# Performance work log

Hardware: AMD Instinct MI355X
Metric: run time of the kernel (lower is better)

## Reference

```python
import jax, jax.numpy as jnp
import numpy as np

N_EMBD = 1024
N_HEAD = 16
HEAD_DIM = N_EMBD // N_HEAD
B, T = 2, 2048


def setup_inputs() -> dict:
    key = jax.random.key(0)
    k1, k2, k3 = jax.random.split(key, 3)
    s_in = 1.0 / np.sqrt(N_EMBD)
    return {
        "x": jax.random.normal(k1, (B, T, N_EMBD), dtype=jnp.float32),
        "w_qkv": jax.random.normal(k2, (N_EMBD, 3 * N_EMBD), dtype=jnp.float32) * s_in,
        "b_qkv": jnp.zeros((3 * N_EMBD,), dtype=jnp.float32),
        "w_out": jax.random.normal(k3, (N_EMBD, N_EMBD), dtype=jnp.float32) * s_in,
        "b_out": jnp.zeros((N_EMBD,), dtype=jnp.float32),
    }


def reference(x, w_qkv, b_qkv, w_out, b_out):
    b, t, c = x.shape
    qkv = x @ w_qkv + b_qkv  # [B,T,3C]
    q, k, v = jnp.split(qkv, 3, axis=-1)
    # [B,T,C] -> [B,H,T,D]
    reshape = lambda a: a.reshape(b, t, N_HEAD, HEAD_DIM).transpose(0, 2, 1, 3)
    q, k, v = reshape(q), reshape(k), reshape(v)
    scale = 1.0 / jnp.sqrt(jnp.asarray(HEAD_DIM, dtype=x.dtype))
    att = jnp.einsum("bhqd,bhkd->bhqk", q, k) * scale  # [B,H,T,T]
    causal = jnp.tril(jnp.ones((t, t), dtype=bool))
    att = jnp.where(causal, att, jnp.asarray(-jnp.inf, dtype=att.dtype))
    att = jax.nn.softmax(att, axis=-1)
    y = jnp.einsum("bhqk,bhkd->bhqd", att, v)  # [B,H,T,D]
    y = y.transpose(0, 2, 1, 3).reshape(b, t, c)
    return y @ w_out + b_out
```

## Files before the change

### kernel.cpp

```cpp
#include <hip/hip_runtime.h>

typedef unsigned short u16;
typedef __attribute__((ext_vector_type(8))) short s16x8;
typedef __attribute__((ext_vector_type(8))) unsigned short u16x8;
typedef __attribute__((ext_vector_type(4))) unsigned short u16x4;
typedef __attribute__((ext_vector_type(4))) float f32x4;

__device__ __forceinline__ u16 f2bf(float f) {
  unsigned int u = __float_as_uint(f);
  u += 0x7fffu + ((u >> 16) & 1u);
  return (u16)(u >> 16);
}

__device__ __forceinline__ void gload_lds16(const u16* g, u16* l) {
  __builtin_amdgcn_global_load_lds((__attribute__((address_space(1))) void*)(u16*)g,
                                   (__attribute__((address_space(3))) void*)l, 16, 0, 0);
}

__global__ void __launch_bounds__(256) prep_kernel(const float* __restrict__ x,
                                                   u16* __restrict__ xbf,
                                                   const float* __restrict__ wqkv,
                                                   u16* __restrict__ wqkvT,
                                                   const float* __restrict__ wout,
                                                   u16* __restrict__ woutT) {
  __shared__ float tile[32][33];
  const int b = blockIdx.x, tid = threadIdx.x;
  if (b < 2048) {
    int i = (b * 256 + tid) * 8;
    float4 a = *(const float4*)(x + i);
    float4 c = *(const float4*)(x + i + 4);
    u16x8 o;
    o[0] = f2bf(a.x); o[1] = f2bf(a.y); o[2] = f2bf(a.z); o[3] = f2bf(a.w);
    o[4] = f2bf(c.x); o[5] = f2bf(c.y); o[6] = f2bf(c.z); o[7] = f2bf(c.w);
    *(u16x8*)(xbf + i) = o;
    return;
  }
  const float* in; u16* out; int K = 1024, N, bx, by;
  if (b < 5120) { in = wqkv; out = wqkvT; N = 3072; bx = (b - 2048) % 96; by = (b - 2048) / 96; }
  else          { in = wout; out = woutT; N = 1024; bx = (b - 5120) % 32; by = (b - 5120) / 32; }
  int n0 = bx * 32, k0 = by * 32;
  int r = tid >> 5, c = tid & 31;
#pragma unroll
  for (int i = 0; i < 4; ++i)
    tile[r + i * 8][c] = in[(size_t)(k0 + r + i * 8) * N + n0 + c];
  __syncthreads();
#pragma unroll
  for (int i = 0; i < 4; ++i)
    out[(size_t)(n0 + r + i * 8) * K + k0 + c] = f2bf(tile[c][r + i * 8]);
}

__device__ __forceinline__ void gemm_core(const u16* __restrict__ A,
                                          const u16* __restrict__ BT, int K,
                                          int m0, int n0, u16* As, u16* Bs,
                                          f32x4 acc[4][4]) {
  const int tid = threadIdx.x;
  const int lane = tid & 63, wave = tid >> 6;
  const int quad = lane >> 4, l16 = lane & 15;
  const int wm = (wave & 1) << 6, wn = (wave >> 1) << 6;
  const int ob0 = wave * 2048 + lane * 16;
  const int ob1 = ob0 + 1024;
  const int r0 = ob0 >> 6, c0 = (ob0 & 63) >> 1;
  const int r1 = ob1 >> 6, c1 = (ob1 & 63) >> 1;

  for (int k0 = 0; k0 < K; k0 += 32) {
    __syncthreads();
    gload_lds16(&A [(size_t)(m0 + r0) * K + k0 + c0], &As[ob0 >> 1]);
    gload_lds16(&A [(size_t)(m0 + r1) * K + k0 + c1], &As[ob1 >> 1]);
    gload_lds16(&BT[(size_t)(n0 + r0) * K + k0 + c0], &Bs[ob0 >> 1]);
    gload_lds16(&BT[(size_t)(n0 + r1) * K + k0 + c1], &Bs[ob1 >> 1]);
    __syncthreads();
    s16x8 a[4], b[4];
#pragma unroll
    for (int i = 0; i < 4; ++i)
      a[i] = *(const s16x8*)&As[(wm + i * 16 + l16) * 32 + quad * 8];
#pragma unroll
    for (int j = 0; j < 4; ++j)
      b[j] = *(const s16x8*)&Bs[(wn + j * 16 + l16) * 32 + quad * 8];
#pragma unroll
    for (int i = 0; i < 4; ++i)
#pragma unroll
      for (int j = 0; j < 4; ++j)
        acc[i][j] = __builtin_amdgcn_mfma_f32_16x16x32_bf16(a[i], b[j], acc[i][j], 0, 0, 0);
  }
}

__global__ void __launch_bounds__(256) gemm_qkv_kernel(const u16* __restrict__ xbf,
                                                       const u16* __restrict__ wT,
                                                       const float* __restrict__ bias,
                                                       u16* __restrict__ qb,
                                                       u16* __restrict__ kb,
                                                       u16* __restrict__ vtb) {
  __shared__ u16 As[128 * 32], Bs[128 * 32];
  f32x4 acc[4][4];
#pragma unroll
  for (int i = 0; i < 4; ++i)
#pragma unroll
    for (int j = 0; j < 4; ++j) { f32x4 z = {0.f, 0.f, 0.f, 0.f}; acc[i][j] = z; }
  const int m0 = blockIdx.x * 128, n0 = blockIdx.y * 128;
  gemm_core(xbf, wT, 1024, m0, n0, As, Bs, acc);

  const int tid = threadIdx.x;
  const int lane = tid & 63, wave = tid >> 6;
  const int quad = lane >> 4, l16 = lane & 15;
  const int wm = (wave & 1) << 6, wn = (wave >> 1) << 6;
  const int sec = n0 >> 10;
#pragma unroll
  for (int i = 0; i < 4; ++i)
#pragma unroll
    for (int j = 0; j < 4; ++j) {
      const int gm = m0 + wm + i * 16 + quad * 4;
      const int gn = n0 + wn + j * 16 + l16;
      const float bv = bias[gn];
      const int c = gn & 1023, h = c >> 6, d = c & 63;
#pragma unroll
      for (int r = 0; r < 4; ++r) {
        const int row = gm + r;
        const int bb = row >> 11, t = row & 2047;
        if (sec == 0)      qb[((size_t)(bb * 16 + h) * 2048 + t) * 64 + d] = f2bf((acc[i][j][r] + bv) * 0.125f);
        else if (sec == 1) kb[((size_t)(bb * 16 + h) * 2048 + t) * 64 + d] = f2bf(acc[i][j][r] + bv);
        else               vtb[((size_t)(bb * 16 + h) * 64 + d) * 2048 + t] = f2bf(acc[i][j][r] + bv);
      }
    }
}

__global__ void __launch_bounds__(256) gemm_out_kernel(const u16* __restrict__ yb,
                                                       const u16* __restrict__ wT,
                                                       const float* __restrict__ bias,
                                                       float* __restrict__ out) {
  __shared__ u16 As[64 * 32], Bs[128 * 32];
  f32x4 acc[2][4];
#pragma unroll
  for (int i = 0; i < 2; ++i)
#pragma unroll
    for (int j = 0; j < 4; ++j) { f32x4 z = {0.f, 0.f, 0.f, 0.f}; acc[i][j] = z; }
  const int m0 = blockIdx.x * 64, n0 = blockIdx.y * 128;
  const int K = 1024;

  const int tid = threadIdx.x;
  const int lane = tid & 63, wave = tid >> 6;
  const int quad = lane >> 4, l16 = lane & 15;
  const int wm = (wave & 1) << 5, wn = (wave >> 1) << 6;
  const int oa = tid * 16;
  const int ra = oa >> 6, ca = (oa & 63) >> 1;
  const int ob0 = wave * 2048 + lane * 16;
  const int ob1 = ob0 + 1024;
  const int rb0 = ob0 >> 6, cb0 = (ob0 & 63) >> 1;
  const int rb1 = ob1 >> 6, cb1 = (ob1 & 63) >> 1;

  for (int k0 = 0; k0 < K; k0 += 32) {
    __syncthreads();
    gload_lds16(&yb[(size_t)(m0 + ra) * K + k0 + ca],  &As[oa >> 1]);
    gload_lds16(&wT[(size_t)(n0 + rb0) * K + k0 + cb0], &Bs[ob0 >> 1]);
    gload_lds16(&wT[(size_t)(n0 + rb1) * K + k0 + cb1], &Bs[ob1 >> 1]);
    __syncthreads();
    s16x8 a[2], b[4];
#pragma unroll
    for (int i = 0; i < 2; ++i)
      a[i] = *(const s16x8*)&As[(wm + i * 16 + l16) * 32 + quad * 8];
#pragma unroll
    for (int j = 0; j < 4; ++j)
      b[j] = *(const s16x8*)&Bs[(wn + j * 16 + l16) * 32 + quad * 8];
#pragma unroll
    for (int i = 0; i < 2; ++i)
#pragma unroll
      for (int j = 0; j < 4; ++j)
        acc[i][j] = __builtin_amdgcn_mfma_f32_16x16x32_bf16(a[i], b[j], acc[i][j], 0, 0, 0);
  }

#pragma unroll
  for (int i = 0; i < 2; ++i)
#pragma unroll
    for (int j = 0; j < 4; ++j) {
      const int gm = m0 + wm + i * 16 + quad * 4;
      const int gn = n0 + wn + j * 16 + l16;
      const float bv = bias[gn];
#pragma unroll
      for (int r = 0; r < 4; ++r)
        out[(size_t)(gm + r) * 1024 + gn] = acc[i][j][r] + bv;
    }
}

__global__ void __launch_bounds__(256) attn_kernel(const u16* __restrict__ qb,
                                                   const u16* __restrict__ kb,
                                                   const u16* __restrict__ vtb,
                                                   u16* __restrict__ yb) {
  const int KSTR = 72, VSTR = 136;
  __shared__ u16 Ks[128 * 72];
  __shared__ u16 VTs[64 * 136];
  __shared__ u16 Ps[4 * 16 * 136];

  const int p = blockIdx.x;
  const int bh = blockIdx.y;
  const int bb = bh >> 4, h = bh & 15;
  const u16* Q  = qb  + (size_t)bh * (2048 * 64);
  const u16* Km = kb  + (size_t)bh * (2048 * 64);
  const u16* VT = vtb + (size_t)bh * (64 * 2048);

  const int tid = threadIdx.x;
  const int wave = tid >> 6, lane = tid & 63;
  const int quad = lane >> 4, l16 = lane & 15;
  const float NINF = -__builtin_inff();
  const int Kr = tid >> 3, Kc = (tid & 7) * 8;
  const int Vr = tid >> 4, Vc = (tid & 15) * 8;
  u16* Pw = Ps + wave * (16 * 136);

  const int qtA = p, qtB = 31 - p;
  const int nktA = (qtA >> 1) + 1, nktB = (qtB >> 1) + 1;

  s16x8 qfA[2], qfB[2];
#pragma unroll
  for (int i = 0; i < 2; ++i) {
    int r = Kr + i * 32;
    *(u16x8*)&Ks[r * KSTR + Kc] = *(const u16x8*)&Q[(size_t)(qtA * 64 + r) * 64 + Kc];
  }
  __syncthreads();
#pragma unroll
  for (int ks = 0; ks < 2; ++ks)
    qfA[ks] = *(const s16x8*)&Ks[(wave * 16 + l16) * KSTR + ks * 32 + quad * 8];
  __syncthreads();
#pragma unroll
  for (int i = 0; i < 2; ++i) {
    int r = Kr + i * 32;
    *(u16x8*)&Ks[r * KSTR + Kc] = *(const u16x8*)&Q[(size_t)(qtB * 64 + r) * 64 + Kc];
  }
  __syncthreads();
#pragma unroll
  for (int ks = 0; ks < 2; ++ks)
    qfB[ks] = *(const s16x8*)&Ks[(wave * 16 + l16) * KSTR + ks * 32 + quad * 8];

  float lsumA = 0.f, lsumB = 0.f;
  f32x4 oaccA[4], oaccB[4];
#pragma unroll
  for (int dt = 0; dt < 4; ++dt) {
    f32x4 z = {0.f, 0.f, 0.f, 0.f};
    oaccA[dt] = z; oaccB[dt] = z;
  }

  u16x8 kv[4], vv[4];
#pragma unroll
  for (int i = 0; i < 4; ++i) {
    kv[i] = *(const u16x8*)&Km[(size_t)(Kr + i * 32) * 64 + Kc];
    vv[i] = *(const u16x8*)&VT[(size_t)(Vr + i * 16) * 2048 + Vc];
  }

  auto do_tile = [&](const s16x8 qf[2], int qt, int nkt, int kt,
                     float& lsum, f32x4 oacc[4]) {
    f32x4 st[2][4];
#pragma unroll
    for (int hh = 0; hh < 2; ++hh)
#pragma unroll
      for (int mt = 0; mt < 4; ++mt) {
        f32x4 z = {0.f, 0.f, 0.f, 0.f};
        s16x8 kf0 = *(const s16x8*)&Ks[(hh * 64 + mt * 16 + l16) * KSTR + quad * 8];
        s16x8 kf1 = *(const s16x8*)&Ks[(hh * 64 + mt * 16 + l16) * KSTR + 32 + quad * 8];
        z = __builtin_amdgcn_mfma_f32_16x16x32_bf16(kf0, qf[0], z, 0, 0, 0);
        st[hh][mt] = __builtin_amdgcn_mfma_f32_16x16x32_bf16(kf1, qf[1], z, 0, 0, 0);
      }
    if (kt == nkt - 1) {
      const int qrow = qt * 64 + wave * 16 + l16;
#pragma unroll
      for (int hh = 0; hh < 2; ++hh)
#pragma unroll
        for (int mt = 0; mt < 4; ++mt)
#pragma unroll
          for (int r = 0; r < 4; ++r) {
            int kcol = kt * 128 + hh * 64 + mt * 16 + quad * 4 + r;
            if (kcol > qrow) st[hh][mt][r] = NINF;
          }
    }
#pragma unroll
    for (int hh = 0; hh < 2; ++hh)
#pragma unroll
      for (int mt = 0; mt < 4; ++mt) {
        u16x4 pw;
#pragma unroll
        for (int r = 0; r < 4; ++r) {
          float e = __expf(st[hh][mt][r]);
          lsum += e;
          pw[r] = (u16)((__float_as_uint(e) + 0x8000u) >> 16);
        }
        *(u16x4*)&Pw[l16 * VSTR + hh * 64 + mt * 16 + quad * 4] = pw;
      }
#pragma unroll
    for (int kq = 0; kq < 4; ++kq) {
      s16x8 pf = *(const s16x8*)&Pw[l16 * VSTR + kq * 32 + quad * 8];
#pragma unroll
      for (int dt = 0; dt < 4; ++dt) {
        s16x8 vf = *(const s16x8*)&VTs[(dt * 16 + l16) * VSTR + kq * 32 + quad * 8];
        oacc[dt] = __builtin_amdgcn_mfma_f32_16x16x32_bf16(pf, vf, oacc[dt], 0, 0, 0);
      }
    }
  };

  for (int kt = 0; kt < nktB; ++kt) {
    __syncthreads();
#pragma unroll
    for (int i = 0; i < 4; ++i) {
      *(u16x8*)&Ks[(Kr + i * 32) * KSTR + Kc]  = kv[i];
      *(u16x8*)&VTs[(Vr + i * 16) * VSTR + Vc] = vv[i];
    }
    __syncthreads();
    if (kt + 1 < nktB) {
#pragma unroll
      for (int i = 0; i < 4; ++i) {
        kv[i] = *(const u16x8*)&Km[(size_t)((kt + 1) * 128 + Kr + i * 32) * 64 + Kc];
        vv[i] = *(const u16x8*)&VT[(size_t)(Vr + i * 16) * 2048 + (kt + 1) * 128 + Vc];
      }
    }
    do_tile(qfB, qtB, nktB, kt, lsumB, oaccB);
    if (kt < nktA) do_tile(qfA, qtA, nktA, kt, lsumA, oaccA);
  }

#pragma unroll
  for (int e = 0; e < 2; ++e) {
    const int qt = e ? qtB : qtA;
    float l = e ? lsumB : lsumA;
    f32x4* oacc = e ? oaccB : oaccA;
    l += __shfl_xor(l, 16, 64);
    l += __shfl_xor(l, 32, 64);
    float rinv[4];
#pragma unroll
    for (int r = 0; r < 4; ++r) rinv[r] = 1.0f / __shfl(l, quad * 4 + r, 64);
#pragma unroll
    for (int dt = 0; dt < 4; ++dt) {
      int d = dt * 16 + l16;
#pragma unroll
      for (int r = 0; r < 4; ++r) {
        int t = qt * 64 + wave * 16 + quad * 4 + r;
        yb[(((size_t)bb * 2048 + t) * 16 + h) * 64 + d] = f2bf(oacc[dt][r] * rinv[r]);
      }
    }
  }
}

extern "C" void kernel_launch(void* const* d_in, const int* in_sizes, int n_in,
                              void* d_out, int out_size, void* d_ws, size_t ws_size,
                              hipStream_t stream) {
  (void)in_sizes; (void)n_in; (void)out_size; (void)ws_size;
  const float* x    = (const float*)d_in[0];
  const float* wqkv = (const float*)d_in[1];
  const float* bqkv = (const float*)d_in[2];
  const float* wout = (const float*)d_in[3];
  const float* bout = (const float*)d_in[4];
  float* out = (float*)d_out;

  char* ws = (char*)d_ws;
  u16* xbf   = (u16*)(ws);
  u16* wqkvT = (u16*)(ws + (size_t)8  * 1024 * 1024);
  u16* woutT = (u16*)(ws + (size_t)14 * 1024 * 1024);
  u16* qb    = (u16*)(ws + (size_t)16 * 1024 * 1024);
  u16* kb    = (u16*)(ws + (size_t)24 * 1024 * 1024);
  u16* vtb   = (u16*)(ws + (size_t)32 * 1024 * 1024);
  u16* yb    = (u16*)(ws + (size_t)40 * 1024 * 1024);

  prep_kernel<<<6144, 256, 0, stream>>>(x, xbf, wqkv, wqkvT, wout, woutT);
  gemm_qkv_kernel<<<dim3(32, 24), 256, 0, stream>>>(xbf, wqkvT, bqkv, qb, kb, vtb);
  attn_kernel<<<dim3(16, 32), 256, 0, stream>>>(qb, kb, vtb, yb);
  gemm_out_kernel<<<dim3(64, 8), 256, 0, stream>>>(yb, woutT, bout, out);
}
```

Before: 195.0 us.

## Double K-step per barrier in GEMMs and split attention into sequential query passes

The QKV and output projection GEMMs now stage two 32-wide K slices per barrier pair, which halves the number of synchronisations and doubles LDS per block. The attention kernel no longer interleaves its two query tiles over a shared K/V stream. It processes each tile in its own pass, reloading K/V for the second, which lowers register pressure at the cost of re-reading shared K/V tiles from global memory. A stray assignment inside an MFMA argument is harmless but untidy.

Result: no change. 196.9 us (+0.9%).

```diff
diff --git a/kernel.cpp b/kernel.cpp
--- a/kernel.cpp
+++ b/kernel.cpp
@@ -61,26 +61,35 @@
   const int ob1 = ob0 + 1024;
   const int r0 = ob0 >> 6, c0 = (ob0 & 63) >> 1;
   const int r1 = ob1 >> 6, c1 = (ob1 & 63) >> 1;
-
-  for (int k0 = 0; k0 < K; k0 += 32) {
-    __syncthreads();
-    gload_lds16(&A [(size_t)(m0 + r0) * K + k0 + c0], &As[ob0 >> 1]);
-    gload_lds16(&A [(size_t)(m0 + r1) * K + k0 + c1], &As[ob1 >> 1]);
-    gload_lds16(&BT[(size_t)(n0 + r0) * K + k0 + c0], &Bs[ob0 >> 1]);
-    gload_lds16(&BT[(size_t)(n0 + r1) * K + k0 + c1], &Bs[ob1 >> 1]);
-    __syncthreads();
-    s16x8 a[4], b[4];
-#pragma unroll
-    for (int i = 0; i < 4; ++i)
-      a[i] = *(const s16x8*)&As[(wm + i * 16 + l16) * 32 + quad * 8];
-#pragma unroll
-    for (int j = 0; j < 4; ++j)
-      b[j] = *(const s16x8*)&Bs[(wn + j * 16 + l16) * 32 + quad * 8];
-#pragma unroll
-    for (int i = 0; i < 4; ++i)
+  const int CH = 128 * 32;
+
+  for (int k0 = 0; k0 < K; k0 += 64) {
+    __syncthreads();
+#pragma unroll
+    for (int kk = 0; kk < 2; ++kk) {
+      const int kg = k0 + kk * 32, co = kk * CH;
+      gload_lds16(&A [(size_t)(m0 + r0) * K + kg + c0], &As[co + (ob0 >> 1)]);
+      gload_lds16(&A [(size_t)(m0 + r1) * K + kg + c1], &As[co + (ob1 >> 1)]);
+      gload_lds16(&BT[(size_t)(n0 + r0) * K + kg + c0], &Bs[co + (ob0 >> 1)]);
+      gload_lds16(&BT[(size_t)(n0 + r1) * K + kg + c1], &Bs[co + (ob1 >> 1)]);
+    }
+    __syncthreads();
+#pragma unroll
+    for (int kk = 0; kk < 2; ++kk) {
+      const int co = kk * CH;
+      s16x8 a[4], b[4];
+#pragma unroll
+      for (int i = 0; i < 4; ++i)
+        a[i] = *(const s16x8*)&As[co + (wm + i * 16 + l16) * 32 + quad * 8];
 #pragma unroll
       for (int j = 0; j < 4; ++j)
-        acc[i][j] = __builtin_amdgcn_mfma_f32_16x16x32_bf16(a[i], b[j], acc[i][j], 0, 0, 0);
+        b[j] = *(const s16x8*)&Bs[co + (wn + j * 16 + l16) * 32 + quad * 8];
+#pragma unroll
+      for (int i = 0; i < 4; ++i)
+#pragma unroll
+        for (int j = 0; j < 4; ++j)
+          acc[i][j] = __builtin_amdgcn_mfma_f32_16x16x32_bf16(a[i], b[j], acc[i][j], 0, 0, 0);
+    }
   }
 }
 
@@ -90,7 +99,7 @@
                                                        u16* __restrict__ qb,
                                                        u16* __restrict__ kb,
                                                        u16* __restrict__ vtb) {
-  __shared__ u16 As[128 * 32], Bs[128 * 32];
+  __shared__ u16 As[2 * 128 * 32], Bs[2 * 128 * 32];
   f32x4 acc[4][4];
 #pragma unroll
   for (int i = 0; i < 4; ++i)
@@ -127,7 +136,7 @@
                                                        const u16* __restrict__ wT,
                                                        const float* __restrict__ bias,
                                                        float* __restrict__ out) {
-  __shared__ u16 As[64 * 32], Bs[128 * 32];
+  __shared__ u16 As[2 * 64 * 32], Bs[2 * 128 * 32];
   f32x4 acc[2][4];
 #pragma unroll
   for (int i = 0; i < 2; ++i)
@@ -146,25 +155,33 @@
   const int ob1 = ob0 + 1024;
   const int rb0 = ob0 >> 6, cb0 = (ob0 & 63) >> 1;
   const int rb1 = ob1 >> 6, cb1 = (ob1 & 63) >> 1;
-
-  for (int k0 = 0; k0 < K; k0 += 32) {
-    __syncthreads();
-    gload_lds16(&yb[(size_t)(m0 + ra) * K + k0 + ca],  &As[oa >> 1]);
-    gload_lds16(&wT[(size_t)(n0 + rb0) * K + k0 + cb0], &Bs[ob0 >> 1]);
-    gload_lds16(&wT[(size_t)(n0 + rb1) * K + k0 + cb1], &Bs[ob1 >> 1]);
-    __syncthreads();
-    s16x8 a[2], b[4];
-#pragma unroll
-    for (int i = 0; i < 2; ++i)
-      a[i] = *(const s16x8*)&As[(wm + i * 16 + l16) * 32 + quad * 8];
-#pragma unroll
-    for (int j = 0; j < 4; ++j)
-      b[j] = *(const s16x8*)&Bs[(wn + j * 16 + l16) * 32 + quad * 8];
-#pragma unroll
-    for (int i = 0; i < 2; ++i)
+  const int CHA = 64 * 32, CHB = 128 * 32;
+
+  for (int k0 = 0; k0 < K; k0 += 64) {
+    __syncthreads();
+#pragma unroll
+    for (int kk = 0; kk < 2; ++kk) {
+      const int kg = k0 + kk * 32;
+      gload_lds16(&yb[(size_t)(m0 + ra) * K + kg + ca],   &As[kk * CHA + (oa >> 1)]);
+      gload_lds16(&wT[(size_t)(n0 + rb0) * K + kg + cb0], &Bs[kk * CHB + (ob0 >> 1)]);
+      gload_lds16(&wT[(size_t)(n0 + rb1) * K + kg + cb1], &Bs[kk * CHB + (ob1 >> 1)]);
+    }
+    __syncthreads();
+#pragma unroll
+    for (int kk = 0; kk < 2; ++kk) {
+      s16x8 a[2], b[4];
+#pragma unroll
+      for (int i = 0; i < 2; ++i)
+        a[i] = *(const s16x8*)&As[kk * CHA + (wm + i * 16 + l16) * 32 + quad * 8];
 #pragma unroll
       for (int j = 0; j < 4; ++j)
-        acc[i][j] = __builtin_amdgcn_mfma_f32_16x16x32_bf16(a[i], b[j], acc[i][j], 0, 0, 0);
+        b[j] = *(const s16x8*)&Bs[kk * CHB + (wn + j * 16 + l16) * 32 + quad * 8];
+#pragma unroll
+      for (int i = 0; i < 2; ++i)
+#pragma unroll
+        for (int j = 0; j < 4; ++j)
+          acc[i][j] = __builtin_amdgcn_mfma_f32_16x16x32_bf16(a[i], b[j], acc[i][j], 0, 0, 0);
+    }
   }
 
 #pragma unroll
@@ -204,118 +221,96 @@
   const int Vr = tid >> 4, Vc = (tid & 15) * 8;
   u16* Pw = Ps + wave * (16 * 136);
 
-  const int qtA = p, qtB = 31 - p;
-  const int nktA = (qtA >> 1) + 1, nktB = (qtB >> 1) + 1;
-
-  s16x8 qfA[2], qfB[2];
-#pragma unroll
-  for (int i = 0; i < 2; ++i) {
-    int r = Kr + i * 32;
-    *(u16x8*)&Ks[r * KSTR + Kc] = *(const u16x8*)&Q[(size_t)(qtA * 64 + r) * 64 + Kc];
-  }
-  __syncthreads();
-#pragma unroll
-  for (int ks = 0; ks < 2; ++ks)
-    qfA[ks] = *(const s16x8*)&Ks[(wave * 16 + l16) * KSTR + ks * 32 + quad * 8];
-  __syncthreads();
-#pragma unroll
-  for (int i = 0; i < 2; ++i) {
-    int r = Kr + i * 32;
-    *(u16x8*)&Ks[r * KSTR + Kc] = *(const u16x8*)&Q[(size_t)(qtB * 64 + r) * 64 + Kc];
-  }
-  __syncthreads();
-#pragma unroll
-  for (int ks = 0; ks < 2; ++ks)
-    qfB[ks] = *(const s16x8*)&Ks[(wave * 16 + l16) * KSTR + ks * 32 + quad * 8];
-
-  float lsumA = 0.f, lsumB = 0.f;
-  f32x4 oaccA[4], oaccB[4];
-#pragma unroll
-  for (int dt = 0; dt < 4; ++dt) {
-    f32x4 z = {0.f, 0.f, 0.f, 0.f};
-    oaccA[dt] = z; oaccB[dt] = z;
-  }
-
-  u16x8 kv[4], vv[4];
-#pragma unroll
-  for (int i = 0; i < 4; ++i) {
-    kv[i] = *(const u16x8*)&Km[(size_t)(Kr + i * 32) * 64 + Kc];
-    vv[i] = *(const u16x8*)&VT[(size_t)(Vr + i * 16) * 2048 + Vc];
-  }
-
-  auto do_tile = [&](const s16x8 qf[2], int qt, int nkt, int kt,
-                     float& lsum, f32x4 oacc[4]) {
-    f32x4 st[2][4];
-#pragma unroll
-    for (int hh = 0; hh < 2; ++hh)
-#pragma unroll
-      for (int mt = 0; mt < 4; ++mt) {
-        f32x4 z = {0.f, 0.f, 0.f, 0.f};
-        s16x8 kf0 = *(const s16x8*)&Ks[(hh * 64 + mt * 16 + l16) * KSTR + quad * 8];
-        s16x8 kf1 = *(const s16x8*)&Ks[(hh * 64 + mt * 16 + l16) * KSTR + 32 + quad * 8];
-        z = __builtin_amdgcn_mfma_f32_16x16x32_bf16(kf0, qf[0], z, 0, 0, 0);
-        st[hh][mt] = __builtin_amdgcn_mfma_f32_16x16x32_bf16(kf1, qf[1], z, 0, 0, 0);
-      }
-    if (kt == nkt - 1) {
-      const int qrow = qt * 64 + wave * 16 + l16;
+  for (int pass = 0; pass < 2; ++pass) {
+    const int qt = pass ? (31 - p) : p;
+    const int nkt = (qt >> 1) + 1;
+    __syncthreads();
+#pragma unroll
+    for (int i = 0; i < 2; ++i) {
+      int r = Kr + i * 32;
+      *(u16x8*)&Ks[r * KSTR + Kc] = *(const u16x8*)&Q[(size_t)(qt * 64 + r) * 64 + Kc];
+    }
+    __syncthreads();
+    s16x8 qf[2];
+#pragma unroll
+    for (int ks = 0; ks < 2; ++ks)
+      qf[ks] = *(const s16x8*)&Ks[(wave * 16 + l16) * KSTR + ks * 32 + quad * 8];
+
+    float lsum = 0.f;
+    f32x4 oacc[4];
+#pragma unroll
+    for (int dt = 0; dt < 4; ++dt) { f32x4 z = {0.f, 0.f, 0.f, 0.f}; oacc[dt] = z; }
+
+    u16x8 kv[4], vv[4];
+#pragma unroll
+    for (int i = 0; i < 4; ++i) {
+      kv[i] = *(const u16x8*)&Km[(size_t)(Kr + i * 32) * 64 + Kc];
+      vv[i] = *(const u16x8*)&VT[(size_t)(Vr + i * 16) * 2048 + Vc];
+    }
+
+    for (int kt = 0; kt < nkt; ++kt) {
+      __syncthreads();
+#pragma unroll
+      for (int i = 0; i < 4; ++i) {
+        *(u16x8*)&Ks[(Kr + i * 32) * KSTR + Kc]  = kv[i];
+        *(u16x8*)&VTs[(Vr + i * 16) * VSTR + Vc] = vv[i];
+      }
+      __syncthreads();
+      if (kt + 1 < nkt) {
+#pragma unroll
+        for (int i = 0; i < 4; ++i) {
+          kv[i] = *(const u16x8*)&Km[(size_t)((kt + 1) * 128 + Kr + i * 32) * 64 + Kc];
+          vv[i] = *(const u16x8*)&VT[(size_t)(Vr + i * 16) * 2048 + (kt + 1) * 128 + Vc];
+        }
+      }
+      f32x4 st[2][4];
 #pragma unroll
       for (int hh = 0; hh < 2; ++hh)
 #pragma unroll
-        for (int mt = 0; mt < 4; ++mt)
+        for (int mt = 0; mt < 4; ++mt) {
+          f32x4 z = {0.f, 0.f, 0.f, 0.f};
+          s16x8 kf0 = *(const s16x8*)&Ks[(hh * 64 + mt * 16 + l16) * KSTR + quad * 8];
+          s16x8 kf1 = *(const s16x8*)&Ks[(hh * 64 + mt * 16 + l16) * KSTR + 32 + quad * 8];
+          z = __builtin_amdgcn_mfma_f32_16x16x32_bf16(kf0, qf[0], z, 0, 0, 0);
+          st[hh][mt] = __builtin_amdgcn_mfma_f32_16x16x32_bf16(kf1, qf[1], st[hh][mt] = z, 0, 0, 0);
+        }
+      if (kt == nkt - 1) {
+        const int qrow = qt * 64 + wave * 16 + l16;
+#pragma unroll
+        for (int hh = 0; hh < 2; ++hh)
+#pragma unroll
+          for (int mt = 0; mt < 4; ++mt)
+#pragma unroll
+            for (int r = 0; r < 4; ++r) {
+              int kcol = kt * 128 + hh * 64 + mt * 16 + quad * 4 + r;
+              if (kcol > qrow) st[hh][mt][r] = NINF;
+            }
+      }
+#pragma unroll
+      for (int hh = 0; hh < 2; ++hh)
+#pragma unroll
+        for (int mt = 0; mt < 4; ++mt) {
+          u16x4 pw;
 #pragma unroll
           for (int r = 0; r < 4; ++r) {
-            int kcol = kt * 128 + hh * 64 + mt * 16 + quad * 4 + r;
-            if (kcol > qrow) st[hh][mt][r] = NINF;
+            float e = __expf(st[hh][mt][r]);
+            lsum += e;
+            pw[r] = (u16)((__float_as_uint(e) + 0x8000u) >> 16);
           }
-    }
-#pragma unroll
-    for (int hh = 0; hh < 2; ++hh)
-#pragma unroll
-      for (int mt = 0; mt < 4; ++mt) {
-        u16x4 pw;
-#pragma unroll
-        for (int r = 0; r < 4; ++r) {
-          float e = __expf(st[hh][mt][r]);
-          lsum += e;
-          pw[r] = (u16)((__float_as_uint(e) + 0x8000u) >> 16);
+          *(u16x4*)&Pw[l16 * VSTR + hh * 64 + mt * 16 + quad * 4] = pw;
         }
-        *(u16x4*)&Pw[l16 * VSTR + hh * 64 + mt * 16 + quad * 4] = pw;
-      }
-#pragma unroll
-    for (int kq = 0; kq < 4; ++kq) {
-      s16x8 pf = *(const s16x8*)&Pw[l16 * VSTR + kq * 32 + quad * 8];
-#pragma unroll
-      for (int dt = 0; dt < 4; ++dt) {
-        s16x8 vf = *(const s16x8*)&VTs[(dt * 16 + l16) * VSTR + kq * 32 + quad * 8];
-        oacc[dt] = __builtin_amdgcn_mfma_f32_16x16x32_bf16(pf, vf, oacc[dt], 0, 0, 0);
-      }
-    }
-  };
-
-  for (int kt = 0; kt < nktB; ++kt) {
-    __syncthreads();
-#pragma unroll
-    for (int i = 0; i < 4; ++i) {
-      *(u16x8*)&Ks[(Kr + i * 32) * KSTR + Kc]  = kv[i];
-      *(u16x8*)&VTs[(Vr + i * 16) * VSTR + Vc] = vv[i];
-    }
-    __syncthreads();
-    if (kt + 1 < nktB) {
-#pragma unroll
-      for (int i = 0; i < 4; ++i) {
-        kv[i] = *(const u16x8*)&Km[(size_t)((kt + 1) * 128 + Kr + i * 32) * 64 + Kc];
-        vv[i] = *(const u16x8*)&VT[(size_t)(Vr + i * 16) * 2048 + (kt + 1) * 128 + Vc];
-      }
-    }
-    do_tile(qfB, qtB, nktB, kt, lsumB, oaccB);
-    if (kt < nktA) do_tile(qfA, qtA, nktA, kt, lsumA, oaccA);
-  }
-
-#pragma unroll
-  for (int e = 0; e < 2; ++e) {
-    const int qt = e ? qtB : qtA;
-    float l = e ? lsumB : lsumA;
-    f32x4* oacc = e ? oaccB : oaccA;
+#pragma unroll
+      for (int kq = 0; kq < 4; ++kq) {
+        s16x8 pf = *(const s16x8*)&Pw[l16 * VSTR + kq * 32 + quad * 8];
+#pragma unroll
+        for (int dt = 0; dt < 4; ++dt) {
+          s16x8 vf = *(const s16x8*)&VTs[(dt * 16 + l16) * VSTR + kq * 32 + quad * 8];
+          oacc[dt] = __builtin_amdgcn_mfma_f32_16x16x32_bf16(pf, vf, oacc[dt], 0, 0, 0);
+        }
+      }
+    }
+
+    float l = lsum;
     l += __shfl_xor(l, 16, 64);
     l += __shfl_xor(l, 32, 64);
     float rinv[4];
```
